# Kernel tuning notes

Hardware: AMD Instinct MI355X
Metric: run time of the kernel (lower is better)

## Reference

```python
import jax, jax.numpy as jnp
import numpy as np

# ---- problem constants (from init_kwargs / grids) ----
R, NX, NV = 64, 32768, 16384
LX, VMAX = 1.0, 8.0
DX = LX / NX
DV = 2.0 * VMAX / NV
DT = 1e-3
AE, AI = 1.0, 1836.0
ZE, ZI = -1.0, 1.0
OMEGA_C_TAU = 1.0
OMEGA_P_TAU = 1.0
NU_E, NU_I = 1.0, 0.04
XS = jnp.asarray((np.arange(NX) + 0.5) * DX - LX / 2, jnp.float32)
VS = jnp.asarray(-VMAX + (np.arange(NV) + 0.5) * DV, jnp.float32)
V_PLUS = jnp.where(VS > 0, VS, 0.0)
V_MINUS = jnp.where(VS < 0, VS, 0.0)
NU_SHAPE = jnp.ones(NX, jnp.float32)                     # collision_frequency_shape_func
_g = jnp.exp(-0.5 * (XS / (0.1 * LX)) ** 2)
GSHAPE = (_g / (jnp.sum(_g) * DX)).astype(jnp.float32)   # flux_source_shape_func


def _maxwellian(A):
    return jnp.sqrt(A / (2.0 * jnp.pi)) * jnp.exp(-A * VS ** 2 / 2.0)


def _pad(K, g):
    # AbsorbingWall: zero ghost cells
    return jnp.pad(K, ((0, 0), (g, g)))


def _dV_mats(V):
    dV = jnp.diff(V, axis=1) / DV
    z = jnp.zeros((R, 1), V.dtype)
    Vl = V @ jnp.concatenate([z, dV], axis=1).T * DV
    Vr = V @ jnp.concatenate([dV, z], axis=1).T * DV
    return Vl, Vr


def _poisson(rho):
    # 1D Gauss law: dE/dx = omega_p_tau^2 * rho_c, zero-mean gauge
    E = OMEGA_P_TAU ** 2 * jnp.cumsum(rho) * DX
    return E - jnp.mean(E)


def _flux_out_ion(Xi, Si, Vi):
    f_edge = (Xi[:, -1] @ Si) @ Vi            # (Nv,)
    return jnp.sum(V_PLUS * f_edge) * DV


def _K_rhs(K, V, E, A, Z, nu0, flux_out):
    vpm = (V_PLUS[None, :] * V) @ V.T * DV    # V @ diag(v+) @ V.T * dv, (r,r)
    vmm = (V_MINUS[None, :] * V) @ V.T * DV
    Vl, Vr = _dV_mats(V)
    Kb = _pad(K, 2)                           # (r, Nx+4)
    # upwind flux at Nx+1 interfaces
    flux = vpm @ Kb[:, 1:-2] + vmm @ Kb[:, 2:-1]
    v_flux_diff = jnp.diff(flux, axis=1) / DX
    fac = OMEGA_C_TAU * Z / A
    Ep = jnp.where(fac * E > 0, fac * E, 0.0)[None, :]
    Em = jnp.where(fac * E < 0, fac * E, 0.0)[None, :]
    E_flux = Vl @ (K * Ep) + Vr @ (K * Em)
    gamma = flux_out * GSHAPE
    n = K.T @ V.sum(1) * DV                   # (Nx,)
    nu = nu0 * NU_SHAPE
    VM = V @ _maxwellian(A) * DV              # (r,)
    coll = (n * nu + gamma)[None, :] * VM[:, None] - K * nu[None, :]
    return -v_flux_diff - E_flux + coll


def _S_rhs(S, X, V, E, A, Z, nu0, flux_out):
    vpm = (V_PLUS[None, :] * V) @ V.T * DV
    vmm = (V_MINUS[None, :] * V) @ V.T * DV
    K = _pad((X.T @ S).T, 1)                  # (r, Nx+2)
    Klm = X @ (jnp.diff(K[:, :-1], axis=1) / DX).T * DX
    Krm = X @ (jnp.diff(K[:, 1:], axis=1) / DX).T * DX
    v_term = Klm @ vpm.T + Krm @ vmm.T
    Vl, Vr = _dV_mats(V)
    fac = OMEGA_C_TAU * Z / A
    Epm = X @ (jnp.where(fac * E > 0, fac * E, 0.0)[:, None] * X.T) * DX
    Emm = X @ (jnp.where(fac * E < 0, fac * E, 0.0)[:, None] * X.T) * DX
    E_term = Epm @ S @ Vl.T + Emm @ S @ Vr.T
    gamma = flux_out * GSHAPE
    n = X.T @ (S @ V.sum(1)) * DV             # (Nx,)
    nu = nu0 * NU_SHAPE
    Xng = X @ (n * nu + gamma) * DX           # (r,)
    Xnm = X @ (nu[:, None] * X.T) * DX
    VM = V @ _maxwellian(A) * DV
    coll = Xng[:, None] * VM[None, :] - Xnm @ S
    return v_term + E_term - coll


def _L_rhs(L, X, E, A, Z, nu0, flux_out):
    Vt, St = jnp.linalg.qr(L.T)
    S = St.T * DV ** 0.5
    V = Vt.T / DV ** 0.5
    K = _pad((X.T @ S).T, 1)
    Klm = X @ (jnp.diff(K[:, :-1], axis=1) / DX).T * DX
    Krm = X @ (jnp.diff(K[:, 1:], axis=1) / DX).T * DX
    v_flux = V_PLUS[None, :] * (Klm @ V) + V_MINUS[None, :] * (Krm @ V)
    fac = OMEGA_C_TAU * Z / A
    Epm = X @ (jnp.where(fac * E > 0, fac * E, 0.0)[:, None] * X.T) * DX
    Emm = X @ (jnp.where(fac * E < 0, fac * E, 0.0)[:, None] * X.T) * DX
    Lb = _pad(L, 2)                           # (r, Nv+4)
    flux = Epm @ Lb[:, 1:-2] + Emm @ Lb[:, 2:-1]   # (r, Nv+1)
    E_flux = jnp.diff(flux, axis=1) / DV
    gamma = flux_out * GSHAPE
    n = X.T @ L.sum(1) * DV
    nu = nu0 * NU_SHAPE
    Xng = X @ (gamma + n * nu) * DX
    Xnm = X @ (nu[:, None] * X.T) * DX
    M = _maxwellian(A)
    coll = Xng[:, None] * M[None, :] - Xnm @ L
    return -v_flux - E_flux + coll


def _forward(Xe, Se, Ve, Xi, Si, Vi):
    # ---- K step (rk1 = forward Euler) ----
    flux_out = _flux_out_ion(Xi, Si, Vi)
    Ke = (Xe.T @ Se).T
    Ki = (Xi.T @ Si).T
    rho = ZE * (Ke.T @ Ve.sum(1)) * DV + ZI * (Ki.T @ Vi.sum(1)) * DV
    E = _poisson(rho)
    Ke = Ke + DT * _K_rhs(Ke, Ve, E, AE, ZE, NU_E, flux_out)
    Ki = Ki + DT * _K_rhs(Ki, Vi, E, AI, ZI, NU_I, flux_out)
    Qe, Re_ = jnp.linalg.qr(Ke.T)
    Xe, Se = Qe.T / DX ** 0.5, Re_ * DX ** 0.5
    Qi, Ri_ = jnp.linalg.qr(Ki.T)
    Xi, Si = Qi.T / DX ** 0.5, Ri_ * DX ** 0.5
    # ---- S step ----
    flux_out = _flux_out_ion(Xi, Si, Vi)
    rho = ZE * (Xe.T @ (Se @ Ve.sum(1))) * DV + ZI * (Xi.T @ (Si @ Vi.sum(1))) * DV
    E = _poisson(rho)
    Se = Se + DT * _S_rhs(Se, Xe, Ve, E, AE, ZE, NU_E, flux_out)
    Si = Si + DT * _S_rhs(Si, Xi, Vi, E, AI, ZI, NU_I, flux_out)
    # ---- L step ----
    flux_out = _flux_out_ion(Xi, Si, Vi)
    Le = Se @ Ve
    Li = Si @ Vi
    rho = ZE * (Xe.T @ Le.sum(1)) * DV + ZI * (Xi.T @ Li.sum(1)) * DV
    E = _poisson(rho)
    Le = Le + DT * _L_rhs(Le, Xe, E, AE, ZE, NU_E, flux_out)
    Li = Li + DT * _L_rhs(Li, Xi, E, AI, ZI, NU_I, flux_out)
    Qe, Re_ = jnp.linalg.qr(Le.T)
    Se, Ve = Re_.T * DV ** 0.5, Qe.T / DV ** 0.5
    Qi, Ri_ = jnp.linalg.qr(Li.T)
    Si, Vi = Ri_.T * DV ** 0.5, Qi.T / DV ** 0.5
    return jnp.stack([jnp.concatenate([Xe, Se, Ve], axis=1),
                      jnp.concatenate([Xi, Si, Vi], axis=1)])


def setup_inputs() -> dict:
    key = jax.random.key(0)
    ks = jax.random.split(key, 6)

    def ortho_x(k):
        Q, _ = jnp.linalg.qr(jax.random.normal(k, (NX, R), jnp.float32))
        return Q.T / DX ** 0.5

    def ortho_v(k):
        Q, _ = jnp.linalg.qr(jax.random.normal(k, (NV, R), jnp.float32))
        return Q.T / DV ** 0.5

    def s_mat(k):
        return 0.1 * jnp.eye(R, dtype=jnp.float32) + 0.01 * jax.random.normal(k, (R, R), jnp.float32)

    return {
        "Xe": ortho_x(ks[0]), "Se": s_mat(ks[1]), "Ve": ortho_v(ks[2]),
        "Xi": ortho_x(ks[3]), "Si": s_mat(ks[4]), "Vi": ortho_v(ks[5]),
    }


def reference(Xe, Se, Ve, Xi, Si, Vi):
    return _forward(Xe, Se, Ve, Xi, Si, Vi)
```

## Files before the change

### kernel.cpp

```cpp
#include <hip/hip_runtime.h>
#include <math.h>

#define NXC 32768
#define NVC 16384
#define OUTWC (NXC + 64 + NVC)

static constexpr float DXf   = 1.0f/32768.0f;
static constexpr float DVf   = 16.0f/16384.0f;
static constexpr float DTf   = 1e-3f;
static constexpr float VMAXf = 8.0f;
static constexpr float INV2PI= 0.15915494309189535f;

#define PS_V 16576
#define PS_X 8256
#define PS_E 8192

__global__ __launch_bounds__(1024) void k_gshape(float* __restrict__ g){
  __shared__ float red[1024];
  int t = threadIdx.x;
  float s = 0.f;
  for (int i = t; i < NXC; i += 1024){
    float x = (i + 0.5f)*DXf - 0.5f;
    float xx = x*10.0f;
    float gv = expf(-0.5f*xx*xx);
    g[i] = gv; s += gv;
  }
  red[t] = s; __syncthreads();
  for (int o = 512; o > 0; o >>= 1){ if (t < o) red[t] += red[t+o]; __syncthreads(); }
  float norm = 1.0f/(red[0]*DXf);
  for (int i = t; i < NXC; i += 1024) g[i] *= norm;
}

__global__ __launch_bounds__(256) void k_vstatsf(const float* __restrict__ V0, const float* __restrict__ V1,
                                                 float* __restrict__ part){
  __shared__ float Vt[64][67];
  int sp = blockIdx.y;
  const float* V = sp ? V1 : V0;
  float Amax = sp ? 1836.0f : 1.0f;
  int blk = blockIdx.x;
  int nbk = gridDim.x;
  int chunk = NVC/nbk;
  int c0b = blk*chunk;
  int tid = threadIdx.x;
  int ta = tid >> 4, tb = tid & 15;
  int a0 = ta*4, b0 = tb*4;
  float acc0[4][4]={{0}}, acc1[4][4]={{0}}, accp[4][4]={{0}}, accm[4][4]={{0}};
  float vsv[4]={0,0,0,0}, vvm[4]={0,0,0,0}, vwv[4]={0,0,0,0};
  float fm = sqrtf(Amax*INV2PI);
  for (int t0 = 0; t0 < chunk; t0 += 64){
    int c0 = c0b + t0;
    for (int i = tid; i < 64*65; i += 256){
      int r = i/65, cc = i%65;
      int c = c0 - 1 + cc;
      Vt[r][cc] = (c >= 0 && c < NVC) ? V[(size_t)r*NVC + c] : 0.f;
    }
    __syncthreads();
    for (int jj = 0; jj < 64; ++jj){
      int j = c0 + jj;
      float vs = -VMAXf + (j + 0.5f)*DVf;
      float wpj = (vs > 0.f ? vs : 0.f)*DVf;
      float wmj = (vs < 0.f ? vs : 0.f)*DVf;
      float av[4], bv[4], bm[4];
      #pragma unroll
      for (int k=0;k<4;k++){ av[k]=Vt[a0+k][jj+1]; bv[k]=Vt[b0+k][jj+1]; bm[k]=Vt[b0+k][jj]; }
      float lag = (j >= 1) ? 1.f : 0.f;
      #pragma unroll
      for (int ka=0;ka<4;ka++){
        #pragma unroll
        for (int kb=0;kb<4;kb++){
          float p = av[ka]*bv[kb];
          acc0[ka][kb] += p;
          accp[ka][kb] += p*wpj;
          accm[ka][kb] += p*wmj;
          acc1[ka][kb] += lag*av[ka]*bm[kb];
        }
      }
      if (tb == 0){
        float mv = fm*expf(-0.5f*Amax*vs*vs)*DVf;
        #pragma unroll
        for (int k=0;k<4;k++){
          vsv[k] += av[k];
          vvm[k] += av[k]*mv;
          vwv[k] += av[k]*wpj;
        }
      }
    }
    __syncthreads();
  }
  float* pb = part + (size_t)(sp*nbk+blk)*PS_V;
  #pragma unroll
  for (int ka=0;ka<4;ka++){
    #pragma unroll
    for (int kb=0;kb<4;kb++){
      int idx = (a0+ka)*64 + (b0+kb);
      pb[idx]        = acc0[ka][kb];
      pb[4096+idx]   = acc1[ka][kb];
      pb[8192+idx]   = accp[ka][kb];
      pb[12288+idx]  = accm[ka][kb];
    }
  }
  if (tb == 0){
    #pragma unroll
    for (int k=0;k<4;k++){
      pb[16384 + a0+k] = vsv[k];
      pb[16448 + a0+k] = vvm[k];
      pb[16512 + a0+k] = vwv[k];
    }
  }
}

__global__ __launch_bounds__(256) void k_xstatsf(const float* __restrict__ X0, const float* __restrict__ X1,
                                                 int pitch, const float* __restrict__ gsh, float* __restrict__ part){
  __shared__ float Xt[64][67];
  int sp = blockIdx.y;
  const float* X = sp ? X1 : X0;
  int blk = blockIdx.x;
  int nbk = gridDim.x;
  int chunk = NXC/nbk;
  int c0b = blk*chunk;
  int tid = threadIdx.x, ta = tid>>4, tb = tid&15, a0 = ta*4, b0 = tb*4;
  float accg[4][4]={{0}}, acch[4][4]={{0}};
  float axg[4]={0,0,0,0};
  for (int t0=0;t0<chunk;t0+=64){
    int c0 = c0b+t0;
    for (int i=tid;i<64*65;i+=256){
      int r=i/65, cc=i%65; int x=c0-1+cc;
      Xt[r][cc] = (x>=0 && x<NXC) ? X[(size_t)r*pitch + x] : 0.f;
    }
    __syncthreads();
    for (int jj=0;jj<64;jj++){
      int x = c0+jj;
      float av[4],bv[4],bm[4];
      #pragma unroll
      for (int k=0;k<4;k++){ av[k]=Xt[a0+k][jj+1]; bv[k]=Xt[b0+k][jj+1]; bm[k]=Xt[b0+k][jj]; }
      float lag = (x>=1)?1.f:0.f;
      #pragma unroll
      for (int ka=0;ka<4;ka++){
        #pragma unroll
        for (int kb=0;kb<4;kb++){
          accg[ka][kb] += av[ka]*bv[kb];
          acch[ka][kb] += lag*av[ka]*bm[kb];
        }
      }
      if (tb==0){
        float gw = gsh[x]*DXf;
        #pragma unroll
        for (int k=0;k<4;k++) axg[k] += av[k]*gw;
      }
    }
    __syncthreads();
  }
  float* pb = part + (size_t)(sp*nbk+blk)*PS_X;
  #pragma unroll
  for (int ka=0;ka<4;ka++){
    #pragma unroll
    for (int kb=0;kb<4;kb++){
      int idx = (a0+ka)*64 + (b0+kb);
      pb[idx] = accg[ka][kb];
      pb[4096+idx] = acch[ka][kb];
    }
  }
  if (tb==0){
    #pragma unroll
    for (int k=0;k<4;k++) pb[8192 + a0+k] = axg[k];
  }
}

__global__ __launch_bounds__(256) void k_eweightf(const float* __restrict__ X0, const float* __restrict__ X1,
                                                  int pitch, const float* __restrict__ E,
                                                  float fac0, float fac1, float* __restrict__ part){
  __shared__ float Xt[64][65];
  __shared__ float Ew[64];
  int sp = blockIdx.y;
  const float* X = sp ? X1 : X0;
  float fac = sp ? fac1 : fac0;
  int blk = blockIdx.x; int chunk = NXC/64; int c0b = blk*chunk;
  int tid = threadIdx.x, ta = tid>>4, tb = tid&15, a0 = ta*4, b0 = tb*4;
  float accp[4][4]={{0}}, accm[4][4]={{0}};
  for (int t0=0;t0<chunk;t0+=64){
    int c0 = c0b+t0;
    for (int i=tid;i<64*64;i+=256){
      int r=i>>6, cc=i&63;
      Xt[r][cc] = X[(size_t)r*pitch + c0+cc];
    }
    if (tid < 64) Ew[tid] = E[c0+tid]*fac;
    __syncthreads();
    for (int jj=0;jj<64;jj++){
      float w0 = Ew[jj];
      float wp = (w0>0.f?w0:0.f)*DXf, wm = (w0<0.f?w0:0.f)*DXf;
      float av[4],bv[4];
      #pragma unroll
      for (int k=0;k<4;k++){ av[k]=Xt[a0+k][jj]; bv[k]=Xt[b0+k][jj]; }
      #pragma unroll
      for (int ka=0;ka<4;ka++){
        #pragma unroll
        for (int kb=0;kb<4;kb++){
          float p = av[ka]*bv[kb];
          accp[ka][kb] += p*wp;
          accm[ka][kb] += p*wm;
        }
      }
    }
    __syncthreads();
  }
  float* pb = part + (size_t)(sp*64+blk)*PS_E;
  #pragma unroll
  for (int ka=0;ka<4;ka++){
    #pragma unroll
    for (int kb=0;kb<4;kb++){
      int idx = (a0+ka)*64 + (b0+kb);
      pb[idx] = accp[ka][kb];
      pb[4096+idx] = accm[ka][kb];
    }
  }
}

__global__ __launch_bounds__(256) void k_reduce32f(const float* __restrict__ part, int nb, int ps,
                                                   float* __restrict__ dst){
  int sp = blockIdx.y;
  int i = blockIdx.x*256 + threadIdx.x;
  if (i < ps){
    float s = 0.f;
    for (int b=0;b<nb;b++) s += part[(size_t)(sp*nb+b)*ps + i];
    dst[(size_t)sp*ps + i] = s;
  }
}

__global__ __launch_bounds__(256) void k_prep1(
  const float* __restrict__ Ve, const float* __restrict__ Vi,
  const float* __restrict__ Se, const float* __restrict__ Si, const float* __restrict__ Xi,
  const float* __restrict__ VDe, const float* __restrict__ VDi,
  float* __restrict__ Vle, float* __restrict__ Vre, float* __restrict__ Vli, float* __restrict__ Vri,
  float* __restrict__ VleT, float* __restrict__ VreT, float* __restrict__ VliT, float* __restrict__ VriT,
  float* __restrict__ ae, float* __restrict__ ai, float* __restrict__ fluxg)
{
  int t = threadIdx.x;
  const float* g0e = VDe; const float* g1e = VDe+4096;
  const float* g0i = VDi; const float* g1i = VDi+4096;
  const float* sVe = VDe+16384; const float* sVi = VDi+16384;
  const float* wvi = VDi+16512;
  for (int i=t;i<4096;i+=256){
    int a=i>>6, b=i&63;
    int it = b*64+a;
    float v0a=Ve[(size_t)a*NVC], v0b=Ve[(size_t)b*NVC];
    float vea=Ve[(size_t)a*NVC+NVC-1], veb=Ve[(size_t)b*NVC+NVC-1];
    float vle = (g0e[i] - v0a*v0b) - g1e[i];
    float vre = g1e[it] - g0e[i] + vea*veb;
    Vle[i] = vle; VleT[it] = vle;
    Vre[i] = vre; VreT[it] = vre;
    float w0a=Vi[(size_t)a*NVC], w0b=Vi[(size_t)b*NVC];
    float wea=Vi[(size_t)a*NVC+NVC-1], web=Vi[(size_t)b*NVC+NVC-1];
    float vli = (g0i[i] - w0a*w0b) - g1i[i];
    float vri = g1i[it] - g0i[i] + wea*web;
    Vli[i] = vli; VliT[it] = vli;
    Vri[i] = vri; VriT[it] = vri;
  }
  __shared__ float red[64];
  if (t < 64){
    float s1=0.f,s2=0.f,tr=0.f;
    for (int q=0;q<64;q++){
      s1 += Se[t*64+q]*sVe[q];
      s2 += Si[t*64+q]*sVi[q];
      tr += Xi[(size_t)q*NXC + (NXC-1)]*Si[q*64+t];
    }
    ae[t]=s1; ai[t]=s2; red[t]=tr*wvi[t];
  }
  __syncthreads();
  if (t==0){ float s=0.f; for (int r=0;r<64;r++) s+=red[r]; fluxg[0]=s; }
}

__global__ __launch_bounds__(256) void k_prep2(const float* __restrict__ Sce, const float* __restrict__ Sci,
    const float* __restrict__ VDe, const float* __restrict__ VDi, const float* __restrict__ XiN,
    const float* __restrict__ XDe, const float* __restrict__ XDi,
    float* __restrict__ ae, float* __restrict__ ai,
    float* __restrict__ Xnge, float* __restrict__ Xngi, float* __restrict__ fluxg)
{
  const float* sVe = VDe+16384; const float* sVi = VDi+16384; const float* wvi = VDi+16512;
  __shared__ float red[64];
  int t=threadIdx.x;
  if (t<64){
    float s1=0.f,s2=0.f,tr=0.f;
    for (int q=0;q<64;q++){
      s1 += Sce[t*64+q]*sVe[q];
      s2 += Sci[t*64+q]*sVi[q];
      tr += XiN[(size_t)q*OUTWC + (NXC-1)]*Sci[q*64+t];
    }
    ae[t]=s1; ai[t]=s2; red[t]=tr*wvi[t];
  }
  __syncthreads();
  if (t==0){ float s=0.f; for(int r=0;r<64;r++) s+=red[r]; fluxg[1]=s; }
  __syncthreads();
  if (t<64){
    float y1=0.f,y2=0.f;
    for (int q=0;q<64;q++){
      y1 += XDe[t*64+q]*ae[q];
      y2 += XDi[t*64+q]*ai[q];
    }
    float f = fluxg[1];
    Xnge[t] = 1.0f *DXf*DVf*y1 + f*XDe[8192+t];
    Xngi[t] = 0.04f*DXf*DVf*y2 + f*XDi[8192+t];
  }
}

__global__ __launch_bounds__(256) void k_prep3(const float* __restrict__ S2e, const float* __restrict__ S2i,
    const float* __restrict__ VDe, const float* __restrict__ VDi, const float* __restrict__ XiN,
    const float* __restrict__ XDe, const float* __restrict__ XDi,
    float* __restrict__ HTe, float* __restrict__ HTi,
    float* __restrict__ ae, float* __restrict__ ai,
    float* __restrict__ Xnge, float* __restrict__ Xngi, float* __restrict__ fluxg)
{
  const float* sVe = VDe+16384; const float* sVi = VDi+16384; const float* wvi = VDi+16512;
  const float* Ge = XDe; const float* Gi = XDi;
  const float* XGe = XDe+8192; const float* XGi = XDi+8192;
  __shared__ float red[64];
  int t=threadIdx.x;
  for (int i=t;i<4096;i+=256){
    int it = (i&63)*64 + (i>>6);
    HTe[it] = XDe[4096+i];
    HTi[it] = XDi[4096+i];
  }
  if (t<64){
    float s1=0.f,s2=0.f,tr=0.f;
    for (int q=0;q<64;q++){
      s1 += S2e[t*64+q]*sVe[q];
      s2 += S2i[t*64+q]*sVi[q];
      tr += XiN[(size_t)q*OUTWC + (NXC-1)]*S2i[q*64+t];
    }
    ae[t]=s1; ai[t]=s2; red[t]=tr*wvi[t];
  }
  __syncthreads();
  if (t==0){ float s=0.f; for(int r=0;r<64;r++) s+=red[r]; fluxg[2]=s; }
  __syncthreads();
  if (t<64){
    float y1=0.f,y2=0.f;
    for (int q=0;q<64;q++){ y1 += Ge[t*64+q]*ae[q]; y2 += Gi[t*64+q]*ai[q]; }
    float f3 = fluxg[2];
    Xnge[t] = 1.0f *DXf*DVf*y1 + f3*XGe[t];
    Xngi[t] = 0.04f*DXf*DVf*y2 + f3*XGi[t];
  }
}

__global__ __launch_bounds__(256) void k_rho(const float* __restrict__ Xe, int pe,
                                             const float* __restrict__ Xi, int pi,
                                             const float* __restrict__ ae, const float* __restrict__ ai,
                                             float* __restrict__ rho){
  int x = blockIdx.x*256 + threadIdx.x;
  float s = 0.f;
  for (int r=0;r<64;r++) s += ai[r]*Xi[(size_t)r*pi + x] - ae[r]*Xe[(size_t)r*pe + x];
  rho[x] = DVf*s;
}

__global__ __launch_bounds__(1024) void k_poisson(const float* __restrict__ rho, float* __restrict__ E){
  __shared__ float wsum[16];
  __shared__ float bsum[16];
  int t = threadIdx.x;
  int base = t*32;
  float loc[32];
  float run = 0.f;
  #pragma unroll
  for (int i=0;i<32;i++){ run += rho[base+i]; loc[i]=run; }
  float v = run;
  for (int off=1; off<64; off<<=1){
    float u = __shfl_up(v, off, 64);
    if ((t&63) >= off) v += u;
  }
  int wave = t>>6;
  if ((t&63)==63) wsum[wave] = v;
  __syncthreads();
  if (t==0){
    float a=0.f;
    for (int w0=0;w0<16;w0++){ float x=wsum[w0]; wsum[w0]=a; a+=x; }
  }
  __syncthreads();
  float offset = wsum[wave] + (v - run);
  float msum = 0.f;
  #pragma unroll
  for (int i=0;i<32;i++){ float e = DXf*(offset + loc[i]); loc[i]=e; msum += e; }
  float rs2 = msum;
  for (int off=32; off>0; off>>=1) rs2 += __shfl_down(rs2, off, 64);
  if ((t&63)==0) bsum[wave]=rs2;
  __syncthreads();
  if (t==0){ float a=0.f; for(int w0=0;w0<16;w0++) a+=bsum[w0]; bsum[0]=a; }
  __syncthreads();
  float mean = bsum[0]/(float)NXC;
  #pragma unroll
  for (int i=0;i<32;i++) E[base+i] = loc[i]-mean;
}

struct KArg { const float *X, *S, *VD, *VlT, *VrT; float nu, fac; float* Kout; };
__global__ __launch_bounds__(256) void k_kstepf(KArg k0, KArg k1,
    const float* __restrict__ E, const float* __restrict__ gsh, const float* __restrict__ fluxg)
{
  KArg A = blockIdx.y ? k1 : k0;
  __shared__ float Sl[64*65];
  __shared__ __align__(16) float Xt[64*36];
  __shared__ __align__(16) float Kt[64*36];
  __shared__ float sVs[64], VMs[64];
  int x0 = blockIdx.x*32;
  int tid = threadIdx.x;
  for (int i=tid;i<4096;i+=256) Sl[(i>>6)*65+(i&63)] = A.S[i];
  for (int i=tid;i<64*36;i+=256){
    int r=i/36, cc=i%36; int x = x0-1+cc;
    Xt[i] = (cc<34 && x>=0 && x<NXC)? A.X[(size_t)r*NXC+x] : 0.f;
  }
  if (tid<64){ sVs[tid]=A.VD[16384+tid]; VMs[tid]=A.VD[16448+tid]; }
  __syncthreads();
  for (int u=tid; u<576; u+=256){
    int q=u/9, cc0=(u%9)*4;
    float ax=0.f, ay=0.f, az=0.f, aw=0.f;
    for (int p=0;p<64;p++){
      float s = Sl[p*65+q];
      float4 xv = *reinterpret_cast<const float4*>(&Xt[p*36+cc0]);
      ax += s*xv.x; ay += s*xv.y; az += s*xv.z; aw += s*xv.w;
    }
    float4 o; o.x=ax; o.y=ay; o.z=az; o.w=aw;
    *reinterpret_cast<float4*>(&Kt[q*36+cc0]) = o;
  }
  __syncthreads();
  int r = tid & 63, w8 = (tid>>6)*8;
  float fo = fluxg[0];
  const float DTDX = DTf/DXf;
  const float* __restrict__ vpmT = A.VD + 8192;
  const float* __restrict__ vmmT = A.VD + 12288;
  const float* __restrict__ VlT  = A.VlT;
  const float* __restrict__ VrT  = A.VrT;
  float acc[8], nacc[8], epv[8], emv[8];
  #pragma unroll
  for (int c=0;c<8;c++){
    int x = x0 + w8 + c;
    float Ex = A.fac*E[x];
    epv[c] = DTf*(Ex>0.f?Ex:0.f); emv[c] = DTf*(Ex<0.f?Ex:0.f);
    acc[c]=0.f; nacc[c]=0.f;
  }
  #pragma unroll 2
  for (int q=0;q<64;q++){
    float vp_ = DTDX*vpmT[q*64+r];
    float vm_ = DTDX*vmmT[q*64+r];
    float vl  = VlT[q*64+r];
    float vr  = VrT[q*64+r];
    float sq  = sVs[q];
    float w0 = vm_ - vp_;
    float kseg[10];
    #pragma unroll
    for (int c=0;c<10;c++) kseg[c] = Kt[q*36 + w8 + c];
    #pragma unroll
    for (int c=0;c<8;c++){
      float kk0 = kseg[c+1];
      float t = w0 - (epv[c]*vl + emv[c]*vr);
      acc[c] += t*kk0 + vp_*kseg[c] - vm_*kseg[c+2];
      nacc[c] += sq*kk0;
    }
  }
  float vmr = VMs[r];
  #pragma unroll
  for (int c=0;c<8;c++){
    int x = x0 + w8 + c;
    float y = Kt[r*36 + w8 + c + 1]*(1.f - DTf*A.nu) + acc[c]
            + DTf*(nacc[c]*DVf*A.nu + fo*gsh[x])*vmr;
    A.Kout[(size_t)r*NXC + x] = y;
  }
}

struct LArg { const float *V, *S2, *ED, *XD, *HT, *Xng; float nu, Amax; float* Lout; };
__global__ __launch_bounds__(256) void k_lstepf(LArg l0, LArg l1)
{
  LArg A = blockIdx.y ? l1 : l0;
  __shared__ float S2l[64*65];
  __shared__ __align__(16) float Vt[64*36];
  __shared__ __align__(16) float Lt[64*36];
  __shared__ float xngs[64];
  int v0 = blockIdx.x*32;
  int tid = threadIdx.x;
  for (int i=tid;i<4096;i+=256) S2l[(i>>6)*65+(i&63)] = A.S2[i];
  for (int i=tid;i<64*36;i+=256){
    int r=i/36, cc=i%36; int vv = v0-1+cc;
    Vt[i] = (cc<34 && vv>=0 && vv<NVC)? A.V[(size_t)r*NVC+vv] : 0.f;
  }
  if (tid<64) xngs[tid]=A.Xng[tid];
  __syncthreads();
  for (int u=tid; u<576; u+=256){
    int rr=u/9, cc0=(u%9)*4;
    float ax=0.f, ay=0.f, az=0.f, aw=0.f;
    for (int q=0;q<64;q++){
      float s = S2l[rr*65+q];
      float4 xv = *reinterpret_cast<const float4*>(&Vt[q*36+cc0]);
      ax += s*xv.x; ay += s*xv.y; az += s*xv.z; aw += s*xv.w;
    }
    float4 o; o.x=ax; o.y=ay; o.z=az; o.w=aw;
    *reinterpret_cast<float4*>(&Lt[rr*36+cc0]) = o;
  }
  __syncthreads();
  int r = tid & 63, w8 = (tid>>6)*8;
  const float DTDV = DTf/DVf;
  const float* __restrict__ G  = A.XD;
  const float* __restrict__ H  = A.XD + 4096;
  const float* __restrict__ HT = A.HT;
  const float* __restrict__ Ep = A.ED;
  const float* __restrict__ Em = A.ED + 4096;
  float fm = sqrtf(A.Amax*INV2PI);
  float acc[8], vpc[8], vmc[8], mvv[8];
  #pragma unroll
  for (int c=0;c<8;c++){
    int vgl = v0 + w8 + c;
    float vs = -VMAXf + (vgl+0.5f)*DVf;
    vpc[c] = vs>0.f?vs:0.f; vmc[c] = vs<0.f?vs:0.f;
    mvv[c] = fm*expf(-0.5f*A.Amax*vs*vs);
    acc[c] = 0.f;
  }
  #pragma unroll 2
  for (int q=0;q<64;q++){
    float g  = G[q*64+r];
    float h  = HT[q*64+r];
    float ht = H[q*64+r];
    float ep = Ep[q*64+r];
    float em = Em[q*64+r];
    float gh = DTf*(g-h), hg = DTf*(ht-g);
    float dep = DTDV*ep, dem = DTDV*em;
    float b0 = -DTf*A.nu*DXf*g - (dep - dem);
    float lseg[10];
    #pragma unroll
    for (int c=0;c<10;c++) lseg[c] = Lt[q*36 + w8 + c];
    #pragma unroll
    for (int c=0;c<8;c++){
      float t = b0 - (vpc[c]*gh + vmc[c]*hg);
      acc[c] += t*lseg[c+1] + dep*lseg[c] - dem*lseg[c+2];
    }
  }
  float xr = xngs[r];
  #pragma unroll
  for (int c=0;c<8;c++){
    int vgl = v0 + w8 + c;
    float y = Lt[r*36 + w8 + c + 1] + acc[c] + DTf*xr*mvv[c];
    A.Lout[(size_t)r*NVC + vgl] = y;
  }
}

struct SPArg { const float *S, *XD, *ED, *Vl, *Vr, *VD; float nu; float* P; };
__global__ __launch_bounds__(256) void k_sprod(SPArg ea, SPArg ia){
  SPArg A = blockIdx.z ? ia : ea;
  int p  = blockIdx.y;
  int r0 = blockIdx.x*16;
  __shared__ float Sl[4096];
  __shared__ float Mb[16*65];
  __shared__ float M2[64*65];
  __shared__ float Tt[16*65];
  int tid = threadIdx.x;
  const float* G  = A.XD;
  const float* H  = A.XD + 4096;
  const float* Ep = A.ED;
  const float* Em = A.ED + 4096;
  for (int i=tid;i<4096;i+=256) Sl[i] = A.S[i];
  for (int i=tid;i<1024;i+=256){
    int rr=i>>6, c=i&63, r=r0+rr;
    float m;
    if      (p==0) m = G[r*64+c]-H[r*64+c];
    else if (p==1) m = H[c*64+r]-G[r*64+c];
    else if (p==2) m = Ep[r*64+c];
    else if (p==3) m = Em[r*64+c];
    else           m = G[r*64+c];
    Mb[rr*65+c]=m;
  }
  __syncthreads();
  int rr = tid>>4, b0 = (tid&15)*4;
  float acc[4]={0.f,0.f,0.f,0.f};
  for (int c=0;c<64;c++){
    float m = Mb[rr*65+c];
    #pragma unroll
    for (int k=0;k<4;k++) acc[k] += m*Sl[c*64+b0+k];
  }
  if (p==4){
    float s = A.nu*DXf;
    #pragma unroll
    for (int k=0;k<4;k++) A.P[(size_t)p*4096 + (r0+rr)*64 + b0+k] = s*acc[k];
    return;
  }
  #pragma unroll
  for (int k=0;k<4;k++) Tt[rr*65+b0+k]=acc[k];
  if (p<2){
    const float* src = (p==0)? A.VD+8192 : A.VD+12288;
    for (int i=tid;i<4096;i+=256){ int c=i>>6,b=i&63; M2[c*65+b]=src[i]; }
  } else {
    const float* src = (p==2)? A.Vl : A.Vr;
    for (int i=tid;i<4096;i+=256){ int b=i>>6,c=i&63; M2[c*65+b]=src[i]; }
  }
  __syncthreads();
  float acc2[4]={0.f,0.f,0.f,0.f};
  for (int c=0;c<64;c++){
    float t = Tt[rr*65+c];
    #pragma unroll
    for (int k=0;k<4;k++) acc2[k] += t*M2[c*65+b0+k];
  }
  #pragma unroll
  for (int k=0;k<4;k++) A.P[(size_t)p*4096 + (r0+rr)*64 + b0+k] = acc2[k];
}

__global__ __launch_bounds__(256) void k_scomb(const float* __restrict__ Se, const float* __restrict__ Si,
    const float* __restrict__ P,
    const float* __restrict__ Xnge, const float* __restrict__ Xngi,
    const float* __restrict__ VDe, const float* __restrict__ VDi,
    float* __restrict__ S2e, float* __restrict__ S2i){
  int sp = blockIdx.y;
  int i = blockIdx.x*256 + threadIdx.x;
  const float* S   = sp ? Si : Se;
  const float* Pb  = P + (size_t)sp*5*4096;
  const float* xng = sp ? Xngi : Xnge;
  const float* VMv = (sp ? VDi : VDe) + 16448;
  float* S2 = sp ? S2i : S2e;
  int a=i>>6, b=i&63;
  float s = ((Pb[i] + Pb[4096+i]) + (Pb[8192+i] + Pb[12288+i])) + Pb[16384+i] - xng[a]*VMv[b];
  S2[i] = S[i] + DTf*s;
}

__global__ __launch_bounds__(256) void k_gramf(const float* __restrict__ A0, const float* __restrict__ A1,
                                               int n, float* __restrict__ part){
  __shared__ float At[64][65];
  int sp = blockIdx.y;
  const float* A = sp ? A1 : A0;
  int blk = blockIdx.x, nb = gridDim.x;
  int chunk = n/nb;
  int c0b = blk*chunk;
  int tid=threadIdx.x, ta=tid>>4, tb=tid&15, a0=ta*4, b0=tb*4;
  float acc[4][4]={{0}};
  for (int t0=0;t0<chunk;t0+=64){
    int c0=c0b+t0;
    for (int i=tid;i<64*64;i+=256){ int r=i>>6, cc=i&63; At[r][cc]=A[(size_t)r*n + c0+cc]; }
    __syncthreads();
    for (int cc=0;cc<64;cc++){
      float av[4],bv[4];
      #pragma unroll
      for(int k=0;k<4;k++){ av[k]=At[a0+k][cc]; bv[k]=At[b0+k][cc]; }
      #pragma unroll
      for(int ka=0;ka<4;ka++){
        #pragma unroll
        for(int kb=0;kb<4;kb++) acc[ka][kb] += av[ka]*bv[kb];
      }
    }
    __syncthreads();
  }
  float* pb = part + (size_t)(sp*nb+blk)*4096;
  #pragma unroll
  for(int ka=0;ka<4;ka++){
    #pragma unroll
    for(int kb=0;kb<4;kb++) pb[(a0+ka)*64 + b0+kb] = acc[ka][kb];
  }
}

__device__ void chol_blk32(float* __restrict__ M, int tid){
  for (int p=0;p<8;p++){
    const int b=8*p;
    if (tid<64){
      float st[8];
      #pragma unroll
      for (int j=0;j<8;j++) st[j] = M[(b+j)*65 + tid];
      #pragma unroll
      for (int kk=0;kk<8;kk++){
        float q[8];
        #pragma unroll
        for (int j=0;j<8;j++) q[j] = __shfl(st[kk], b+j, 64);
        float d = q[kk];
        float rinv = (d > 0.f) ? 1.f/d : 0.f;
        float sk = st[kk];
        #pragma unroll
        for (int j=0;j<8;j++) if (j>kk) st[j] -= q[j]*sk*rinv;
        st[kk] = sk * ((d > 0.f)? rsqrtf(d) : 0.f);
      }
      #pragma unroll
      for (int j=0;j<8;j++) M[(b+j)*65 + tid] = st[j];
    }
    __syncthreads();
    if (b+8 < 64){
      for (int i=(b+8)*64 + tid; i<4096; i+=512){
        int r=i>>6, c=i&63;
        if (c>=r){
          float s=0.f;
          #pragma unroll
          for (int j=0;j<8;j++) s += M[(b+j)*65+r]*M[(b+j)*65+c];
          M[r*65+c] -= s;
        }
      }
    }
    __syncthreads();
  }
}

struct QArgs {
  const float* Gd; const float* A; int n;
  float scaleS, invQ;
  float* SolveM; float* Sout; int outPitch; int mode;
};
__global__ __launch_bounds__(512) void k_qr(QArgs q0, QArgs q1){
  QArgs Q = (blockIdx.x==0)? q0 : q1;
  __shared__ float Lg[64*65];
  __shared__ float Lw[64*65];
  __shared__ float T[64*65];
  __shared__ float TmpI[448];
  __shared__ float Dv[64];
  int tid = threadIdx.x;
  for (int i=tid;i<4096;i+=512) Lg[(i>>6)*65 + (i&63)] = Q.Gd[i];
  for (int i=tid;i<4096;i+=512){ int c=i>>6, r=i&63; T[r*65+c] = Q.A[(size_t)c*Q.n + r]; }
  __syncthreads();
  chol_blk32(Lg, tid);
  if (tid<64){
    int p=tid>>3, cc=tid&7, b=8*p;
    float wcol[8];
    #pragma unroll
    for (int r=7;r>=0;r--){
      float s = (r==cc)? 1.f : 0.f;
      #pragma unroll
      for (int j=0;j<8;j++) if (j>r) s -= Lg[(b+r)*65 + (b+j)]*wcol[j];
      float dg = Lg[(b+r)*65 + (b+r)];
      wcol[r] = (r<=cc && dg!=0.f)? s/dg : 0.f;
    }
    #pragma unroll
    for (int r=0;r<8;r++) Lw[(b+r)*65 + (b+cc)] = wcol[r];
  }
  __syncthreads();
  for (int d=1; d<8; d++){
    int nb2 = 8-d;
    if (tid < nb2*64){
      int bb=tid>>6, rc=tid&63, r=rc>>3, c=rc&7;
      int p=bb, qb=p+d;
      float s=0.f;
      for (int m=p+1;m<=qb;m++){
        #pragma unroll
        for (int jj=0;jj<8;jj++)
          s += Lg[(8*p+r)*65 + 8*m+jj]*Lw[(8*m+jj)*65 + 8*qb+c];
      }
      TmpI[tid]=s;
    }
    __syncthreads();
    if (tid < nb2*64){
      int bb=tid>>6, rc=tid&63, r=rc>>3, c=rc&7;
      int p=bb, qb=p+d;
      float s=0.f;
      #pragma unroll
      for (int rr=0;rr<8;rr++)
        s += Lw[(8*p+r)*65 + 8*p+rr]*TmpI[(bb<<6)+(rr<<3)+c];
      Lw[(8*p+r)*65 + 8*qb+c] = -s;
    }
    __syncthreads();
  }
  {
    int g = tid>>6, c = tid&63;
    int rbase = g*8;
    for (int k=0;k<64;k++){
      if (tid==k){
        float alpha = T[k*65+k];
        float Ckk = Lg[k*65+k];
        float beta = (alpha>=0.f)? -Ckk : Ckk;
        Dv[k] = (beta>=0.f)? 1.f : -1.f;
      }
      if (rbase+7 > k){
        float alpha = T[k*65+k];
        float Ckk = Lg[k*65+k];
        float beta = (alpha>=0.f)? -Ckk : Ckk;
        float vvh = Ckk*Ckk - alpha*beta;
        float ivv = (vvh>0.f)? __builtin_amdgcn_rcpf(vvh) : 0.f;
        float f = (Lg[k*65+c]*Ckk - beta*T[k*65+c])*ivv;
        if (c > k){
          #pragma unroll
          for (int j=0;j<8;j++){
            int r = rbase+j;
            if (r > k) T[r*65+c] -= f*T[r*65+k];
          }
        }
      }
      __syncthreads();
    }
  }
  for (int i=tid;i<4096;i+=512){
    int r=i>>6, q2=i&63;
    Q.SolveM[i] = (q2<=r)? (Dv[r]*Lw[q2*65+r]*Q.invQ) : 0.f;
    if (Q.mode==0){
      Q.Sout[i] = (q2>=r)? (Dv[r]*Lg[r*65+q2]*Q.scaleS) : 0.f;
    } else {
      Q.Sout[(size_t)r*Q.outPitch + q2] = (r>=q2)? (Dv[q2]*Lg[q2*65+r]*Q.scaleS) : 0.f;
    }
  }
}

__global__ __launch_bounds__(256) void k_qformf(const float* __restrict__ A0, const float* __restrict__ A1,
    int n, const float* __restrict__ M0, const float* __restrict__ M1,
    float* __restrict__ O0, float* __restrict__ O1, int pitch)
{
  int sp = blockIdx.y >> 2;
  const float* A = sp ? A1 : A0;
  const float* M = sp ? M1 : M0;
  float* Out = sp ? O1 : O0;
  int x = blockIdx.x*256 + threadIdx.x;
  int r0 = (blockIdx.y & 3)*16;
  float acc[16];
  #pragma unroll
  for (int rr=0;rr<16;rr++) acc[rr]=0.f;
  for (int q=0;q<64;q++){
    float aq = A[(size_t)q*n + x];
    #pragma unroll
    for (int rr=0;rr<16;rr++) acc[rr] += M[(r0+rr)*64 + q]*aq;
  }
  #pragma unroll
  for (int rr=0;rr<16;rr++) Out[(size_t)(r0+rr)*pitch + x] = acc[rr];
}

extern "C" void kernel_launch(void* const* d_in, const int* in_sizes, int n_in,
                              void* d_out, int out_size, void* d_ws, size_t ws_size,
                              hipStream_t stream)
{
  (void)in_sizes; (void)n_in; (void)out_size; (void)ws_size;
  const float* Xe = (const float*)d_in[0];
  const float* Se = (const float*)d_in[1];
  const float* Ve = (const float*)d_in[2];
  const float* Xi = (const float*)d_in[3];
  const float* Si = (const float*)d_in[4];
  const float* Vi = (const float*)d_in[5];
  float* out = (float*)d_out;
  float* w = (float*)d_ws;

  size_t o = 0;
  auto alloc = [&](size_t nn){ size_t r=o; o += (nn+63)&~(size_t)63; return r; };
  size_t F_VD = alloc(2*PS_V);
  size_t F_XD = alloc(2*PS_X);
  size_t F_ED = alloc(2*PS_E);
  size_t F_VL_E = alloc(4096), F_VR_E = alloc(4096), F_VL_I = alloc(4096), F_VR_I = alloc(4096);
  size_t F_VLT_E = alloc(4096), F_VRT_E = alloc(4096), F_VLT_I = alloc(4096), F_VRT_I = alloc(4096);
  size_t F_HT_E = alloc(4096), F_HT_I = alloc(4096);
  size_t F_SC_E = alloc(4096), F_SC_I = alloc(4096), F_S2_E = alloc(4096), F_S2_I = alloc(4096);
  size_t F_SOLVE_E = alloc(4096), F_SOLVE_I = alloc(4096);
  size_t F_AE = alloc(64), F_AI = alloc(64), F_XNGE = alloc(64), F_XNGI = alloc(64);
  size_t F_FLUX = alloc(64);
  size_t F_GSH = alloc(NXC);
  size_t F_RHO = alloc(NXC);
  size_t F_E   = alloc(NXC);
  size_t F_KE = alloc((size_t)64*NXC);
  size_t F_KI = alloc((size_t)64*NXC);
  size_t F_LE = F_KE;
  size_t F_LI = F_KI;
  size_t F_PART = alloc(1060864);
  size_t F_GQR = alloc(16384);
  float* Gqr = w + F_GQR;
  float* part = w + F_PART;
  float* vpart = w + F_KE;
  float* xpart = w + F_KE;
  float* Pbuf  = w + F_KE;
  const float* VDe = w + F_VD;
  const float* VDi = w + F_VD + PS_V;
  const float* XDe = w + F_XD;
  const float* XDi = w + F_XD + PS_X;
  const float* EDe = w + F_ED;
  const float* EDi = w + F_ED + PS_E;

  float sqDX = sqrtf(DXf), isqDX = 1.f/sqrtf(DXf);
  float sqDV = sqrtf(DVf), isqDV = 1.f/sqrtf(DVf);
  const float NUE = 1.0f, NUI = 0.04f;
  const float FACE = -1.0f, FACI = 1.0f/1836.0f;

  k_vstatsf<<<dim3(128,2),256,0,stream>>>(Ve, Vi, vpart);
  k_reduce32f<<<dim3((PS_V+255)/256,2),256,0,stream>>>(vpart, 128, PS_V, w+F_VD);
  k_gshape<<<1,1024,0,stream>>>(w+F_GSH);
  k_prep1<<<1,256,0,stream>>>(Ve, Vi, Se, Si, Xi, VDe, VDi,
                              w+F_VL_E, w+F_VR_E, w+F_VL_I, w+F_VR_I,
                              w+F_VLT_E, w+F_VRT_E, w+F_VLT_I, w+F_VRT_I,
                              w+F_AE, w+F_AI, w+F_FLUX);
  k_rho<<<NXC/256,256,0,stream>>>(Xe, NXC, Xi, NXC, w+F_AE, w+F_AI, w+F_RHO);
  k_poisson<<<1,1024,0,stream>>>(w+F_RHO, w+F_E);
  KArg ke{Xe, Se, VDe, w+F_VLT_E, w+F_VRT_E, NUE, FACE, w+F_KE};
  KArg ki{Xi, Si, VDi, w+F_VLT_I, w+F_VRT_I, NUI, FACI, w+F_KI};
  k_kstepf<<<dim3(NXC/32,2),256,0,stream>>>(ke, ki, w+F_E, w+F_GSH, w+F_FLUX);
  k_gramf<<<dim3(128,2),256,0,stream>>>(w+F_KE, w+F_KI, NXC, part);
  k_reduce32f<<<dim3(16,2),256,0,stream>>>(part, 128, 4096, Gqr);
  {
    QArgs qe{Gqr,        w+F_KE, NXC, sqDX, isqDX, w+F_SOLVE_E, w+F_SC_E, 0, 0};
    QArgs qi{Gqr+4096,   w+F_KI, NXC, sqDX, isqDX, w+F_SOLVE_I, w+F_SC_I, 0, 0};
    k_qr<<<2,512,0,stream>>>(qe, qi);
  }
  k_qformf<<<dim3(NXC/256,8),256,0,stream>>>(w+F_KE, w+F_KI, NXC, w+F_SOLVE_E, w+F_SOLVE_I,
                                             out, out + (size_t)64*OUTWC, OUTWC);
  k_xstatsf<<<dim3(128,2),256,0,stream>>>(out, out + (size_t)64*OUTWC, OUTWC, w+F_GSH, xpart);
  k_reduce32f<<<dim3((PS_X+255)/256,2),256,0,stream>>>(xpart, 128, PS_X, w+F_XD);
  k_prep2<<<1,256,0,stream>>>(w+F_SC_E, w+F_SC_I, VDe, VDi, out + (size_t)64*OUTWC,
                              XDe, XDi,
                              w+F_AE, w+F_AI, w+F_XNGE, w+F_XNGI, w+F_FLUX);
  k_rho<<<NXC/256,256,0,stream>>>(out, OUTWC, out + (size_t)64*OUTWC, OUTWC, w+F_AE, w+F_AI, w+F_RHO);
  k_poisson<<<1,1024,0,stream>>>(w+F_RHO, w+F_E);
  k_eweightf<<<dim3(64,2),256,0,stream>>>(out, out + (size_t)64*OUTWC, OUTWC, w+F_E, FACE, FACI, part);
  k_reduce32f<<<dim3((PS_E+255)/256,2),256,0,stream>>>(part, 64, PS_E, w+F_ED);
  {
    SPArg spe{w+F_SC_E, XDe, EDe, w+F_VL_E, w+F_VR_E, VDe, NUE, Pbuf};
    SPArg spi{w+F_SC_I, XDi, EDi, w+F_VL_I, w+F_VR_I, VDi, NUI, Pbuf + 5*4096};
    k_sprod<<<dim3(4,5,2),256,0,stream>>>(spe, spi);
  }
  k_scomb<<<dim3(16,2),256,0,stream>>>(w+F_SC_E, w+F_SC_I, Pbuf, w+F_XNGE, w+F_XNGI,
                                       VDe, VDi, w+F_S2_E, w+F_S2_I);
  k_prep3<<<1,256,0,stream>>>(w+F_S2_E, w+F_S2_I, VDe, VDi, out + (size_t)64*OUTWC,
                              XDe, XDi, w+F_HT_E, w+F_HT_I,
                              w+F_AE, w+F_AI, w+F_XNGE, w+F_XNGI, w+F_FLUX);
  k_rho<<<NXC/256,256,0,stream>>>(out, OUTWC, out + (size_t)64*OUTWC, OUTWC, w+F_AE, w+F_AI, w+F_RHO);
  k_poisson<<<1,1024,0,stream>>>(w+F_RHO, w+F_E);
  k_eweightf<<<dim3(64,2),256,0,stream>>>(out, out + (size_t)64*OUTWC, OUTWC, w+F_E, FACE, FACI, part);
  k_reduce32f<<<dim3((PS_E+255)/256,2),256,0,stream>>>(part, 64, PS_E, w+F_ED);
  LArg le{Ve, w+F_S2_E, EDe, XDe, w+F_HT_E, w+F_XNGE, NUE, 1.0f,    w+F_LE};
  LArg li{Vi, w+F_S2_I, EDi, XDi, w+F_HT_I, w+F_XNGI, NUI, 1836.0f, w+F_LI};
  k_lstepf<<<dim3(NVC/32,2),256,0,stream>>>(le, li);
  k_gramf<<<dim3(128,2),256,0,stream>>>(w+F_LE, w+F_LI, NVC, part);
  k_reduce32f<<<dim3(16,2),256,0,stream>>>(part, 128, 4096, Gqr);
  {
    QArgs qe{Gqr,      w+F_LE, NVC, sqDV, isqDV, w+F_SOLVE_E, out + NXC,                        OUTWC, 1};
    QArgs qi{Gqr+4096, w+F_LI, NVC, sqDV, isqDV, w+F_SOLVE_I, out + (size_t)64*OUTWC + NXC,     OUTWC, 1};
    k_qr<<<2,512,0,stream>>>(qe, qi);
  }
  k_qformf<<<dim3(NVC/256,8),256,0,stream>>>(w+F_LE, w+F_LI, NVC, w+F_SOLVE_E, w+F_SOLVE_I,
                                             out + NXC + 64, out + (size_t)64*OUTWC + NXC + 64, OUTWC);
}
```

Measured before the change: 915.8 us.

## Double eweight grid, vectorize shared-memory segment loads, restructure vstats tile load

Doubles the k_eweightf grid to 128 blocks per species, which halves each block's chunk. Its partials now go to a scratch buffer aliased on the K workspace, and the reduction sums 128 partials. The K-step and L-step inner loops now read their 10-element shared-memory segments as float4/float4/float2 vector loads instead of scalar loads. The vstats tile load gains a leftover one-iteration loop that stores the same first element a second time, which adds redundant work. The vector loads depend on 16-byte alignment of the q*36+w8 offsets, and the aliased partial buffer must not overlap data still in use.

```diff
diff --git a/kernel.cpp b/kernel.cpp
--- a/kernel.cpp
+++ b/kernel.cpp
@@ -47,12 +47,23 @@
   float acc0[4][4]={{0}}, acc1[4][4]={{0}}, accp[4][4]={{0}}, accm[4][4]={{0}};
   float vsv[4]={0,0,0,0}, vvm[4]={0,0,0,0}, vwv[4]={0,0,0,0};
   float fm = sqrtf(Amax*INV2PI);
+  int r0s = tid/65, c0s = tid%65;
   for (int t0 = 0; t0 < chunk; t0 += 64){
     int c0 = c0b + t0;
-    for (int i = tid; i < 64*65; i += 256){
-      int r = i/65, cc = i%65;
-      int c = c0 - 1 + cc;
-      Vt[r][cc] = (c >= 0 && c < NVC) ? V[(size_t)r*NVC + c] : 0.f;
+    {
+      int r = r0s, cc = c0s;
+      for (int i = tid; i < 64*65; i += 256){
+        int c = c0 - 1 + cc;
+        Vt[r][cc] = (c >= 0 && c < NVC) ? V[(size_t)r*NVC + c] : 0.f;
+        cc += 256 - 65*3; r += 3;
+        if (cc >= 65){ }
+        break;
+      }
+      for (int i = tid; i < 64*65; i += 256){
+        int rr = i/65, ccc = i%65;
+        int c = c0 - 1 + ccc;
+        Vt[rr][ccc] = (c >= 0 && c < NVC) ? V[(size_t)rr*NVC + c] : 0.f;
+      }
     }
     __syncthreads();
     for (int jj = 0; jj < 64; ++jj){
@@ -174,7 +185,10 @@
   int sp = blockIdx.y;
   const float* X = sp ? X1 : X0;
   float fac = sp ? fac1 : fac0;
-  int blk = blockIdx.x; int chunk = NXC/64; int c0b = blk*chunk;
+  int blk = blockIdx.x;
+  int nbk = gridDim.x;
+  int chunk = NXC/nbk;
+  int c0b = blk*chunk;
   int tid = threadIdx.x, ta = tid>>4, tb = tid&15, a0 = ta*4, b0 = tb*4;
   float accp[4][4]={{0}}, accm[4][4]={{0}};
   for (int t0=0;t0<chunk;t0+=64){
@@ -203,7 +217,7 @@
     }
     __syncthreads();
   }
-  float* pb = part + (size_t)(sp*64+blk)*PS_E;
+  float* pb = part + (size_t)(sp*nbk+blk)*PS_E;
   #pragma unroll
   for (int ka=0;ka<4;ka++){
     #pragma unroll
@@ -440,9 +454,10 @@
     float vr  = VrT[q*64+r];
     float sq  = sVs[q];
     float w0 = vm_ - vp_;
-    float kseg[10];
-    #pragma unroll
-    for (int c=0;c<10;c++) kseg[c] = Kt[q*36 + w8 + c];
+    const float4 kA = *reinterpret_cast<const float4*>(&Kt[q*36 + w8]);
+    const float4 kB = *reinterpret_cast<const float4*>(&Kt[q*36 + w8 + 4]);
+    const float2 kC = *reinterpret_cast<const float2*>(&Kt[q*36 + w8 + 8]);
+    float kseg[10] = {kA.x,kA.y,kA.z,kA.w,kB.x,kB.y,kB.z,kB.w,kC.x,kC.y};
     #pragma unroll
     for (int c=0;c<8;c++){
       float kk0 = kseg[c+1];
@@ -517,9 +532,10 @@
     float gh = DTf*(g-h), hg = DTf*(ht-g);
     float dep = DTDV*ep, dem = DTDV*em;
     float b0 = -DTf*A.nu*DXf*g - (dep - dem);
-    float lseg[10];
-    #pragma unroll
-    for (int c=0;c<10;c++) lseg[c] = Lt[q*36 + w8 + c];
+    const float4 lA = *reinterpret_cast<const float4*>(&Lt[q*36 + w8]);
+    const float4 lB = *reinterpret_cast<const float4*>(&Lt[q*36 + w8 + 4]);
+    const float2 lC = *reinterpret_cast<const float2*>(&Lt[q*36 + w8 + 8]);
+    float lseg[10] = {lA.x,lA.y,lA.z,lA.w,lB.x,lB.y,lB.z,lB.w,lC.x,lC.y};
     #pragma unroll
     for (int c=0;c<8;c++){
       float t = b0 - (vpc[c]*gh + vmc[c]*hg);
@@ -840,6 +856,7 @@
   float* part = w + F_PART;
   float* vpart = w + F_KE;
   float* xpart = w + F_KE;
+  float* epart = w + F_KE;
   float* Pbuf  = w + F_KE;
   const float* VDe = w + F_VD;
   const float* VDi = w + F_VD + PS_V;
@@ -881,8 +898,8 @@
                               w+F_AE, w+F_AI, w+F_XNGE, w+F_XNGI, w+F_FLUX);
   k_rho<<<NXC/256,256,0,stream>>>(out, OUTWC, out + (size_t)64*OUTWC, OUTWC, w+F_AE, w+F_AI, w+F_RHO);
   k_poisson<<<1,1024,0,stream>>>(w+F_RHO, w+F_E);
-  k_eweightf<<<dim3(64,2),256,0,stream>>>(out, out + (size_t)64*OUTWC, OUTWC, w+F_E, FACE, FACI, part);
-  k_reduce32f<<<dim3((PS_E+255)/256,2),256,0,stream>>>(part, 64, PS_E, w+F_ED);
+  k_eweightf<<<dim3(128,2),256,0,stream>>>(out, out + (size_t)64*OUTWC, OUTWC, w+F_E, FACE, FACI, epart);
+  k_reduce32f<<<dim3((PS_E+255)/256,2),256,0,stream>>>(epart, 128, PS_E, w+F_ED);
   {
     SPArg spe{w+F_SC_E, XDe, EDe, w+F_VL_E, w+F_VR_E, VDe, NUE, Pbuf};
     SPArg spi{w+F_SC_I, XDi, EDi, w+F_VL_I, w+F_VR_I, VDi, NUI, Pbuf + 5*4096};
@@ -895,8 +912,8 @@
                               w+F_AE, w+F_AI, w+F_XNGE, w+F_XNGI, w+F_FLUX);
   k_rho<<<NXC/256,256,0,stream>>>(out, OUTWC, out + (size_t)64*OUTWC, OUTWC, w+F_AE, w+F_AI, w+F_RHO);
   k_poisson<<<1,1024,0,stream>>>(w+F_RHO, w+F_E);
-  k_eweightf<<<dim3(64,2),256,0,stream>>>(out, out + (size_t)64*OUTWC, OUTWC, w+F_E, FACE, FACI, part);
-  k_reduce32f<<<dim3((PS_E+255)/256,2),256,0,stream>>>(part, 64, PS_E, w+F_ED);
+  k_eweightf<<<dim3(128,2),256,0,stream>>>(out, out + (size_t)64*OUTWC, OUTWC, w+F_E, FACE, FACI, epart);
+  k_reduce32f<<<dim3((PS_E+255)/256,2),256,0,stream>>>(epart, 128, PS_E, w+F_ED);
   LArg le{Ve, w+F_S2_E, EDe, XDe, w+F_HT_E, w+F_XNGE, NUE, 1.0f,    w+F_LE};
   LArg li{Vi, w+F_S2_I, EDi, XDi, w+F_HT_I, w+F_XNGI, NUI, 1836.0f, w+F_LI};
   k_lstepf<<<dim3(NVC/32,2),256,0,stream>>>(le, li);
```

Result: faster. 889.4 us (-2.9%).
